# Optimization experiments

Hardware: AMD Instinct MI355X
Metric: run time of the kernel (lower is better)

## Reference

```python
import jax, jax.numpy as jnp
import numpy as np

E = 1024
H = 16
DH = E // H
EPS = 1e-8
GRAM_W = 1.5


def _gram_scores(q, k1, k2):
    # q: [BH, L, D], k1/k2: [BH, S, D] -> [BH, L, S]
    ll = jnp.sum(q * q, -1)[:, :, None]          # [BH, L, 1]
    vv = jnp.sum(k1 * k1, -1)[:, None, :]        # [BH, 1, S]
    aa = jnp.sum(k2 * k2, -1)[:, None, :]
    va = jnp.sum(k1 * k2, -1)[:, None, :]
    lv = jnp.einsum('bld,bsd->bls', q, k1)
    la = jnp.einsum('bld,bsd->bls', q, k2)
    det = ll * (vv * aa - va * va) - lv * (lv * aa - la * va) + la * (lv * va - la * vv)
    return -jnp.sqrt(jnp.clip(det, EPS, None))


def setup_inputs() -> dict:
    key = jax.random.key(0)
    ks = jax.random.split(key, 20)
    L, B, S = 512, 4, 1024
    inp = {
        'query': jax.random.normal(ks[0], (L, B, E), jnp.float32),
        'mod1': jax.random.normal(ks[1], (S, B, E), jnp.float32),
        'mod2': jax.random.normal(ks[2], (S, B, E), jnp.float32),
    }
    # Linear params stored as [in, out] (y = x @ W + b), 8 linears
    names = ['q', 'k1', 'k2', 'v1', 'v2', 'g1', 'g2', 'o']
    for i, n in enumerate(names):
        inp[n + '_w'] = jax.random.normal(ks[3 + 2 * i], (E, E), jnp.float32) * 0.02
        inp[n + '_b'] = jax.random.normal(ks[4 + 2 * i], (E,), jnp.float32) * 0.02
    return inp


def reference(query, mod1, mod2,
              q_w, q_b, k1_w, k1_b, k2_w, k2_b, v1_w, v1_b, v2_w, v2_b,
              g1_w, g1_b, g2_w, g2_b, o_w, o_b):
    L, B, _ = query.shape
    S = mod1.shape[0]
    scaling = DH ** -0.5

    def lin(x, w, b):
        return x @ w + b

    def split_heads(x, n):  # [n, B, E] -> [B*H, n, DH]
        return x.reshape(n, B * H, DH).transpose(1, 0, 2)

    q = split_heads(lin(query, q_w, q_b) * scaling, L)
    k1 = split_heads(lin(mod1, k1_w, k1_b), S)
    k2 = split_heads(lin(mod2, k2_w, k2_b), S)
    v1 = split_heads(lin(mod1, v1_w, v1_b), S)
    v2 = split_heads(lin(mod2, v2_w, v2_b), S)

    w1 = jnp.einsum('bld,bsd->bls', q, k1)
    w2 = jnp.einsum('bld,bsd->bls', q, k2)
    gram = _gram_scores(q, k1, k2)
    logits = GRAM_W * gram + w1 + w2          # [BH, L, S]
    attn = jax.nn.softmax(logits, axis=-1)

    def merge_heads(x):  # [B*H, L, DH] -> [L, B, E]
        return x.transpose(1, 0, 2).reshape(L, B, E)

    out1 = merge_heads(jnp.einsum('bls,bsd->bld', attn, v1))
    out2 = merge_heads(jnp.einsum('bls,bsd->bld', attn, v2))
    gate1 = jax.nn.sigmoid(lin(query, g1_w, g1_b))
    gate2 = jax.nn.sigmoid(lin(query, g2_w, g2_b))
    attn_output = lin((out1 * gate1 + out2 * gate2) / 2.0, o_w, o_b)
    avg_weights = attn.reshape(B, H, L, S).mean(axis=1)
    return attn_output, avg_weights
```

## Files before the change

kernel.cpp:

```cpp
#include <hip/hip_runtime.h>
#include <cstddef>
#include <cstdint>

typedef unsigned short ushort_t;
typedef unsigned int uint_t;
typedef __attribute__((ext_vector_type(8))) short short8;
typedef __attribute__((ext_vector_type(4))) float f32x4;

#define EDIM 1024
#define NHEAD 16
#define HDIM 64
#define NB 4
#define LQ 512
#define SK 1024
#define BHD 64

__device__ __forceinline__ ushort_t f2b(float f) {
    uint_t u = __float_as_uint(f);
    return (ushort_t)((u + 0x7fffu + ((u >> 16) & 1u)) >> 16);
}
__device__ __forceinline__ float b2f(ushort_t b) {
    return __uint_as_float(((uint_t)b) << 16);
}

__device__ __forceinline__ void gload_lds16(const void* g, void* l) {
    __builtin_amdgcn_global_load_lds((const __attribute__((address_space(1))) void*)g,
                                     (__attribute__((address_space(3))) void*)l, 16, 0, 0);
}

struct MegaArgs {
    const ushort_t *qx, *m1h, *m1l, *m2h, *m2l;
    const ushort_t *Wqg, *Wkv1, *Wkv2, *Wk1l, *Wk2l;
    const float *q_b, *k1_b, *k2_b, *v1_b, *v2_b, *g1_b, *g2_b;
    float *K1f, *K2f;
    ushort_t *V1b, *V2b, *Qb, *G1b, *G2b;
};

__global__ __launch_bounds__(256, 2)
void mega_gemm(MegaArgs a)
{
    __shared__ ushort_t As[128 * 64];
    __shared__ ushort_t Bs[128 * 64];
    const int tid = threadIdx.x;
    const int wave = tid >> 6, lane = tid & 63;
    const int ln = lane & 15, lq = lane >> 4;
    const int wm = wave & 1, wn = wave >> 1;
    const int mrl = lane >> 3;
    const int lswz = (lane & 7) ^ mrl;

    const int id = blockIdx.x;
    f32x4 zero = {0.f, 0.f, 0.f, 0.f};

    if (id < 512) {
        const int kind = id >> 8;
        const int t = id & 255;
        const int u = t >> 3;
        const int col0 = (u >> 2) * 128;
        const int row0 = ((t & 7) * 4 + (u & 3)) * 128;
        const ushort_t* Ah  = kind ? a.m2h : a.m1h;
        const ushort_t* Alo = kind ? a.m2l : a.m1l;
        const ushort_t* Bh  = kind ? a.Wkv2 : a.Wkv1;
        const ushort_t* Blo = kind ? a.Wk2l : a.Wk1l;
        const float* bias = kind ? a.k2_b : a.k1_b;

        f32x4 acc[4][4];
#pragma unroll
        for (int i = 0; i < 4; ++i)
#pragma unroll
            for (int j = 0; j < 4; ++j) acc[i][j] = zero;

        const int ksub = (lswz & 3) * 8;
        const ushort_t* Asrc = (lswz & 4) ? Alo : Ah;
        const ushort_t* Bsrc = (lswz & 4) ? Blo : Bh;

        for (int kk = 0; kk < 1024; kk += 32) {
            __syncthreads();
#pragma unroll
            for (int j = 0; j < 4; ++j) {
                const int mr = (wave * 4 + j) * 8 + mrl;
                gload_lds16(Asrc + (size_t)(row0 + mr) * 1024 + kk + ksub,
                            (void*)(As + (wave * 4 + j) * 512));
                gload_lds16(Bsrc + (size_t)(col0 + mr) * 1024 + kk + ksub,
                            (void*)(Bs + (wave * 4 + j) * 512));
            }
            __syncthreads();
            short8 ah[4], alv[4], bh[4], blv[4];
#pragma unroll
            for (int i = 0; i < 4; ++i) {
                const int ml = wm * 64 + i * 16 + ln;
                const int pa = (lq ^ (ml & 7)) * 8;
                ah[i]  = *(const short8*)(As + ml * 64 + pa);
                alv[i] = *(const short8*)(As + ml * 64 + (pa ^ 32));
                const int nl = wn * 64 + i * 16 + ln;
                const int pb = (lq ^ (nl & 7)) * 8;
                bh[i]  = *(const short8*)(Bs + nl * 64 + pb);
                blv[i] = *(const short8*)(Bs + nl * 64 + (pb ^ 32));
            }
#pragma unroll
            for (int i = 0; i < 4; ++i)
#pragma unroll
                for (int j = 0; j < 4; ++j)
                    acc[i][j] = __builtin_amdgcn_mfma_f32_16x16x32_bf16(ah[i], bh[j], acc[i][j], 0, 0, 0);
#pragma unroll
            for (int i = 0; i < 4; ++i)
#pragma unroll
                for (int j = 0; j < 4; ++j)
                    acc[i][j] = __builtin_amdgcn_mfma_f32_16x16x32_bf16(ah[i], blv[j], acc[i][j], 0, 0, 0);
#pragma unroll
            for (int i = 0; i < 4; ++i)
#pragma unroll
                for (int j = 0; j < 4; ++j)
                    acc[i][j] = __builtin_amdgcn_mfma_f32_16x16x32_bf16(alv[i], bh[j], acc[i][j], 0, 0, 0);
        }

        float* Y = kind ? a.K2f : a.K1f;
#pragma unroll
        for (int i = 0; i < 4; ++i) {
#pragma unroll
            for (int r = 0; r < 4; ++r) {
                const int row = row0 + wm * 64 + i * 16 + lq * 4 + r;
#pragma unroll
                for (int j = 0; j < 4; ++j) {
                    const int col = col0 + wn * 64 + j * 16 + ln;
                    const float v = acc[i][j][r] + bias[col];
                    const int s = row >> 2, b = row & 3, h = col >> 6, d = col & 63;
                    Y[(((size_t)(b * 16 + h)) * 1024 + s) * 64 + d] = v;
                }
            }
        }
        return;
    }

    int kind, row0, col0;
    const ushort_t *A, *B;
    const float* bias;
    if (id < 1024) {
        int t = id - 512; kind = 2 + (t >> 8); t &= 255;
        const int u = t >> 3;
        col0 = (u >> 2) * 128;
        row0 = ((t & 7) * 4 + (u & 3)) * 128;
        A = (kind == 2) ? a.m1h : a.m2h;
        B = ((kind == 2) ? a.Wkv1 : a.Wkv2) + (size_t)1024 * 1024;
        bias = (kind == 2) ? a.v1_b : a.v2_b;
    } else {
        const int t = id - 1024; kind = 4;
        const int u = t >> 3;
        const int c = (t & 7) * 3 + (u >> 4);
        const int rr = u & 15;
        col0 = c * 128; row0 = rr * 128;
        A = a.qx; B = a.Wqg;
        const int seg = c >> 3;
        bias = (seg == 0) ? a.q_b : ((seg == 1) ? a.g1_b : a.g2_b);
    }

    f32x4 acc[4][4];
#pragma unroll
    for (int i = 0; i < 4; ++i)
#pragma unroll
        for (int j = 0; j < 4; ++j) acc[i][j] = zero;

    for (int kk = 0; kk < 1024; kk += 64) {
        __syncthreads();
#pragma unroll
        for (int j = 0; j < 4; ++j) {
            const int mr = (wave * 4 + j) * 8 + mrl;
            gload_lds16(A + (size_t)(row0 + mr) * 1024 + kk + lswz * 8,
                        (void*)(As + (wave * 4 + j) * 512));
            gload_lds16(B + (size_t)(col0 + mr) * 1024 + kk + lswz * 8,
                        (void*)(Bs + (wave * 4 + j) * 512));
        }
        __syncthreads();
#pragma unroll
        for (int sub = 0; sub < 2; ++sub) {
            short8 af[4], bfv[4];
#pragma unroll
            for (int i = 0; i < 4; ++i) {
                const int ml = wm * 64 + i * 16 + ln;
                af[i] = *(const short8*)(As + ml * 64 + (((sub * 4 + lq) ^ (ml & 7)) * 8));
                const int nl = wn * 64 + i * 16 + ln;
                bfv[i] = *(const short8*)(Bs + nl * 64 + (((sub * 4 + lq) ^ (nl & 7)) * 8));
            }
#pragma unroll
            for (int i = 0; i < 4; ++i)
#pragma unroll
                for (int j = 0; j < 4; ++j)
                    acc[i][j] = __builtin_amdgcn_mfma_f32_16x16x32_bf16(af[i], bfv[j], acc[i][j], 0, 0, 0);
        }
    }

#pragma unroll
    for (int i = 0; i < 4; ++i) {
#pragma unroll
        for (int r = 0; r < 4; ++r) {
            const int row = row0 + wm * 64 + i * 16 + lq * 4 + r;
#pragma unroll
            for (int j = 0; j < 4; ++j) {
                const int col = col0 + wn * 64 + j * 16 + ln;
                const int lc = col & 1023;
                float v = acc[i][j][r] + bias[lc];
                if (kind <= 3) {
                    const int s = row >> 2, b = row & 3, h = lc >> 6, d = lc & 63;
                    ushort_t* Y = (kind == 2) ? a.V1b : a.V2b;
                    Y[(((size_t)(b * 16 + h)) * 1024 + s) * 64 + d] = f2b(v);
                } else {
                    const int seg = col >> 10;
                    if (seg == 0) {
                        v *= 0.125f;
                        const int s = row >> 2, b = row & 3, h = lc >> 6, d = lc & 63;
                        a.Qb[(((size_t)(b * 16 + h)) * 512 + s) * 64 + d] = f2b(v);
                    } else {
                        v = 1.0f / (1.0f + __expf(-v));
                        ushort_t* Y = (seg == 1) ? a.G1b : a.G2b;
                        Y[(size_t)row * 1024 + lc] = f2b(v);
                    }
                }
            }
        }
    }
}

struct CastArgs {
    const float* q; const float* m1; const float* m2;
    ushort_t* qx; ushort_t* m1h; ushort_t* m1l; ushort_t* m2h; ushort_t* m2l;
    const float* wsrc[8];
    ushort_t* whi[8];
    ushort_t* wlo[8];
};

__global__ __launch_bounds__(256)
void casts_kernel(CastArgs a)
{
    __shared__ float T[64][65];
    const int id = blockIdx.x;
    const int tid = threadIdx.x;
    if (id < 1024) {
        const size_t i = ((size_t)id * 256 + tid) * 8;
        float4 x = *(const float4*)(a.q + i);
        float4 y = *(const float4*)(a.q + i + 4);
        ushort_t o[8] = {f2b(x.x), f2b(x.y), f2b(x.z), f2b(x.w), f2b(y.x), f2b(y.y), f2b(y.z), f2b(y.w)};
        *(uint4*)( (void*)(a.qx + i) ) = *(const uint4*)o;
    } else if (id < 5120) {
        const int t = id - 1024;
        const int which = t >> 11;
        const float* x = which ? a.m2 : a.m1;
        ushort_t* yh = which ? a.m2h : a.m1h;
        ushort_t* yl = which ? a.m2l : a.m1l;
        const size_t i = ((size_t)(t & 2047) * 256 + tid) * 8;
        float v[8];
        *(float4*)v = *(const float4*)(x + i);
        *(float4*)(v + 4) = *(const float4*)(x + i + 4);
        ushort_t oh[8], ol[8];
#pragma unroll
        for (int k = 0; k < 8; ++k) {
            oh[k] = f2b(v[k]);
            ol[k] = f2b(v[k] - b2f(oh[k]));
        }
        *(uint4*)( (void*)(yh + i) ) = *(const uint4*)oh;
        *(uint4*)( (void*)(yl + i) ) = *(const uint4*)ol;
    } else {
        const int t = id - 5120;
        const int z = t >> 8, x = t & 15, y = (t >> 4) & 15;
        const float* W = a.wsrc[z];
        ushort_t* Th = a.whi[z];
        ushort_t* Tl = a.wlo[z];
        const int k0 = x * 64, n0 = y * 64;
        const int r = tid >> 2, cg = (tid & 3) * 16;
#pragma unroll
        for (int u = 0; u < 4; ++u) {
            float4 v = *(const float4*)(W + (size_t)(k0 + r) * 1024 + n0 + cg + u * 4);
            T[r][cg + u * 4 + 0] = v.x; T[r][cg + u * 4 + 1] = v.y;
            T[r][cg + u * 4 + 2] = v.z; T[r][cg + u * 4 + 3] = v.w;
        }
        __syncthreads();
        ushort_t oh[16], ol[16];
#pragma unroll
        for (int u = 0; u < 16; ++u) {
            float v = T[cg + u][r];
            oh[u] = f2b(v);
            ol[u] = f2b(v - b2f(oh[u]));
        }
        ushort_t* dh = Th + (size_t)(n0 + r) * 1024 + k0 + cg;
        *(uint4*)( (void*)dh ) = *(const uint4*)oh;
        *(uint4*)( (void*)(dh + 8) ) = *(const uint4*)(oh + 8);
        if (Tl) {
            ushort_t* dl = Tl + (size_t)(n0 + r) * 1024 + k0 + cg;
            *(uint4*)( (void*)dl ) = *(const uint4*)ol;
            *(uint4*)( (void*)(dl + 8) ) = *(const uint4*)(ol + 8);
        }
    }
}

__global__ __launch_bounds__(256)
void prep_kernel(const float* __restrict__ K1f, const float* __restrict__ K2f,
                 ushort_t* __restrict__ K1b, ushort_t* __restrict__ K2b,
                 float* __restrict__ vv, float* __restrict__ aa,
                 float* __restrict__ va2, float* __restrict__ gg,
                 const ushort_t* __restrict__ Qb, float* __restrict__ ll,
                 const ushort_t* __restrict__ V1b, const ushort_t* __restrict__ V2b,
                 ushort_t* __restrict__ V1t, ushort_t* __restrict__ V2t)
{
    __shared__ float T[64][65];
    const int id = blockIdx.x;
    const int tid = threadIdx.x;
    const int wave = tid >> 6, lane = tid & 63;
    if (id < 16384) {
        const int row = id * 4 + wave;
        const float x1 = K1f[(size_t)row * 64 + lane];
        const float x2 = K2f[(size_t)row * 64 + lane];
        K1b[(size_t)row * 64 + lane] = f2b(x1);
        K2b[(size_t)row * 64 + lane] = f2b(x2);
        float s1 = x1 * x1, s2 = x2 * x2, s3 = x1 * x2;
#pragma unroll
        for (int o = 1; o < 64; o <<= 1) {
            s1 += __shfl_xor(s1, o);
            s2 += __shfl_xor(s2, o);
            s3 += __shfl_xor(s3, o);
        }
        if (lane == 0) {
            vv[row] = s1; aa[row] = s2;
            va2[row] = 2.0f * s3;
            gg[row] = s1 * s2 - s3 * s3;
        }
    } else if (id < 24576) {
        const int row = (id - 16384) * 4 + wave;
        const float x = b2f(Qb[(size_t)row * 64 + lane]);
        float s = x * x;
#pragma unroll
        for (int o = 1; o < 64; o <<= 1) s += __shfl_xor(s, o);
        if (lane == 0) ll[row] = s;
    } else {
        const int t = id - 24576;
        const int z = t >> 10, bh = (t >> 4) & 63, s0 = (t & 15) * 64;
        const ushort_t* S = z ? V2b : V1b;
        ushort_t* D = z ? V2t : V1t;
        const int r = tid >> 2, cg = (tid & 3) * 16;
        ushort_t buf[16];
        const ushort_t* sp = S + ((size_t)bh * 1024 + s0 + r) * 64 + cg;
        *(uint4*)buf = *(const uint4*)sp;
        *(uint4*)(buf + 8) = *(const uint4*)(sp + 8);
#pragma unroll
        for (int u = 0; u < 16; ++u) T[r][cg + u] = b2f(buf[u]);
        __syncthreads();
        ushort_t o[16];
#pragma unroll
        for (int u = 0; u < 16; ++u) o[u] = f2b(T[cg + u][r]);
        ushort_t* d = D + ((size_t)bh * 64 + r) * 1024 + s0 + cg;
        *(uint4*)( (void*)d ) = *(const uint4*)o;
        *(uint4*)( (void*)(d + 8) ) = *(const uint4*)(o + 8);
    }
}

__global__ __launch_bounds__(256, 2)
void attn_fused(const ushort_t* __restrict__ Qb, const ushort_t* __restrict__ K1b,
                const ushort_t* __restrict__ K2b, const float* __restrict__ ll,
                const float* __restrict__ vv, const float* __restrict__ aa,
                const float* __restrict__ va2, const float* __restrict__ gg,
                ushort_t* __restrict__ attn, float* __restrict__ C)
{
    __shared__ ushort_t Qs[64 * 64];
    __shared__ ushort_t K1s[128 * 64];
    __shared__ ushort_t K2s[128 * 64];
    __shared__ float vvS[1024], aaS[1024], vaS[1024], ggS[1024], llS[64];
    const int tid = threadIdx.x;
    const int wave = tid >> 6, lane = tid & 63;
    const int ln = lane & 15, lq = lane >> 4;
    const int mrl = lane >> 3;
    const int cswz = (lane & 7) ^ mrl;
    const float L2E = 1.44269504f;

    const int id = blockIdx.x;
    const int bh = (id & 7) * 8 + ((id >> 3) & 7);
    const int l0 = (id >> 6) * 64;

    for (int i = tid; i < 1024; i += 256) {
        vvS[i] = vv[(size_t)bh * 1024 + i];
        aaS[i] = aa[(size_t)bh * 1024 + i];
        vaS[i] = va2[(size_t)bh * 1024 + i];
        ggS[i] = gg[(size_t)bh * 1024 + i];
    }
    if (tid < 64) llS[tid] = ll[(size_t)bh * 512 + l0 + tid];
#pragma unroll
    for (int j = 0; j < 2; ++j) {
        const int mr = (wave * 2 + j) * 8 + mrl;
        gload_lds16(Qb + ((size_t)bh * 512 + l0 + mr) * 64 + cswz * 8,
                    (void*)(Qs + (wave * 2 + j) * 512));
    }

    const int ml = wave * 16 + ln;
    const size_t rb = (size_t)bh * 512 + l0 + wave * 16 + lq * 4;

    float m_run[4], s_run[4];
#pragma unroll
    for (int r = 0; r < 4; ++r) { m_run[r] = -3.0e38f; s_run[r] = 0.f; }
    float mt[8][4];

#pragma unroll
    for (int t = 0; t < 8; ++t) {
        const int s0 = t * 128;
        __syncthreads();
#pragma unroll
        for (int j = 0; j < 4; ++j) {
            const int mr = (wave * 4 + j) * 8 + mrl;
            gload_lds16(K1b + ((size_t)bh * 1024 + s0 + mr) * 64 + cswz * 8,
                        (void*)(K1s + (wave * 4 + j) * 512));
            gload_lds16(K2b + ((size_t)bh * 1024 + s0 + mr) * 64 + cswz * 8,
                        (void*)(K2s + (wave * 4 + j) * 512));
        }
        __syncthreads();
        f32x4 zero = {0.f, 0.f, 0.f, 0.f};
        f32x4 lv[8], la[8];
#pragma unroll
        for (int j = 0; j < 8; ++j) { lv[j] = zero; la[j] = zero; }
#pragma unroll
        for (int sub = 0; sub < 2; ++sub) {
            const short8 qf = *(const short8*)(Qs + ml * 64 + (((sub * 4 + lq) ^ (ml & 7)) * 8));
#pragma unroll
            for (int j = 0; j < 8; ++j) {
                const int nl = j * 16 + ln;
                const short8 k1f = *(const short8*)(K1s + nl * 64 + (((sub * 4 + lq) ^ (nl & 7)) * 8));
                const short8 k2f = *(const short8*)(K2s + nl * 64 + (((sub * 4 + lq) ^ (nl & 7)) * 8));
                lv[j] = __builtin_amdgcn_mfma_f32_16x16x32_bf16(qf, k1f, lv[j], 0, 0, 0);
                la[j] = __builtin_amdgcn_mfma_f32_16x16x32_bf16(qf, k2f, la[j], 0, 0, 0);
            }
        }
        float lgt[8][4];
#pragma unroll
        for (int j = 0; j < 8; ++j) {
            const int c = s0 + j * 16 + ln;
            const float VV = vvS[c], AA = aaS[c], VA2 = vaS[c], GB = ggS[c];
#pragma unroll
            for (int r = 0; r < 4; ++r) {
                const float LL = llS[wave * 16 + lq * 4 + r];
                const float LV = lv[j][r], LA = la[j][r];
                float det = LL * GB;
                det = fmaf(-AA, LV * LV, det);
                det = fmaf(VA2, LV * LA, det);
                det = fmaf(-VV, LA * LA, det);
                det = fmaxf(det, 1e-8f);
                lgt[j][r] = (LV + LA) - 1.5f * sqrtf(det);
            }
        }
        float tmax[4];
#pragma unroll
        for (int r = 0; r < 4; ++r) tmax[r] = lgt[0][r];
#pragma unroll
        for (int j = 1; j < 8; ++j)
#pragma unroll
            for (int r = 0; r < 4; ++r) tmax[r] = fmaxf(tmax[r], lgt[j][r]);
#pragma unroll
        for (int r = 0; r < 4; ++r) {
#pragma unroll
            for (int o = 1; o < 16; o <<= 1) tmax[r] = fmaxf(tmax[r], __shfl_xor(tmax[r], o));
        }
        float mn[4], nm[4], ps[4];
#pragma unroll
        for (int r = 0; r < 4; ++r) {
            mn[r] = fmaxf(m_run[r], tmax[r]);
            nm[r] = -mn[r] * L2E;
            ps[r] = 0.f;
        }
#pragma unroll
        for (int j = 0; j < 8; ++j) {
            const int col = s0 + j * 16 + ln;
            float p[4];
#pragma unroll
            for (int r = 0; r < 4; ++r) {
                p[r] = exp2f(fmaf(lgt[j][r], L2E, nm[r]));
                ps[r] += p[r];
            }
            attn[(rb + 0) * 1024 + col] = f2b(p[0]);
            attn[(rb + 1) * 1024 + col] = f2b(p[1]);
            attn[(rb + 2) * 1024 + col] = f2b(p[2]);
            attn[(rb + 3) * 1024 + col] = f2b(p[3]);
        }
#pragma unroll
        for (int r = 0; r < 4; ++r) {
            s_run[r] = s_run[r] * __expf(m_run[r] - mn[r]) + ps[r];
            m_run[r] = mn[r];
            mt[t][r] = mn[r];
        }
    }

    float inv[4];
#pragma unroll
    for (int r = 0; r < 4; ++r) {
        float s = s_run[r];
#pragma unroll
        for (int o = 1; o < 16; o <<= 1) s += __shfl_xor(s, o);
        inv[r] = 1.0f / s;
    }

    if (ln == 0) {
#pragma unroll
        for (int t = 0; t < 8; ++t) {
#pragma unroll
            for (int r = 0; r < 4; ++r)
                C[(rb + r) * 8 + t] = __expf(mt[t][r] - m_run[r]) * inv[r];
        }
    }
}

__global__ __launch_bounds__(256, 2)
void pv_gate_kernel(const ushort_t* __restrict__ attn, const ushort_t* __restrict__ V1t,
                    const ushort_t* __restrict__ V2t, const ushort_t* __restrict__ G1,
                    const ushort_t* __restrict__ G2, const float* __restrict__ C,
                    ushort_t* __restrict__ tmpb, float* __restrict__ avg)
{
    __shared__ ushort_t Ps[128 * 64];
    __shared__ ushort_t V1s[64 * 64];
    __shared__ ushort_t V2s[64 * 64];
    const int tid = threadIdx.x;

    if (blockIdx.x >= 256) {
        const int t = blockIdx.x - 256;
        const int b = t >> 9, l = t & 511;
        const int c0 = tid * 4;
        const int tt = tid >> 5;
        float s0_ = 0.f, s1_ = 0.f, s2_ = 0.f, s3_ = 0.f;
#pragma unroll
        for (int h = 0; h < 16; ++h) {
            const size_t row = ((size_t)(b * 16 + h)) * 512 + l;
            const float ch = C[row * 8 + tt];
            const ushort_t* p = attn + row * 1024 + c0;
            ushort_t u[4];
            *(uint2*)u = *(const uint2*)p;
            s0_ = fmaf(b2f(u[0]), ch, s0_); s1_ = fmaf(b2f(u[1]), ch, s1_);
            s2_ = fmaf(b2f(u[2]), ch, s2_); s3_ = fmaf(b2f(u[3]), ch, s3_);
        }
        float4 o = {s0_ * 0.0625f, s1_ * 0.0625f, s2_ * 0.0625f, s3_ * 0.0625f};
        *(float4*)(avg + ((size_t)(b * 512 + l)) * 1024 + c0) = o;
        return;
    }

    const int wave = tid >> 6, lane = tid & 63;
    const int ln = lane & 15, lq = lane >> 4;
    const int bh = blockIdx.x >> 2;
    const int l0 = (blockIdx.x & 3) * 128;
    const int cswz = (lane & 7) ^ ((lane >> 3) & 7);
    const int mrl = lane >> 3;
    const int bq = bh >> 4, h = bh & 15;

    f32x4 zero = {0.f, 0.f, 0.f, 0.f};
    f32x4 acc1[2][4], acc2[2][4], tacc1[2][4], tacc2[2][4];
#pragma unroll
    for (int i = 0; i < 2; ++i)
#pragma unroll
        for (int j = 0; j < 4; ++j) {
            acc1[i][j] = zero; acc2[i][j] = zero;
            tacc1[i][j] = zero; tacc2[i][j] = zero;
        }

    for (int s0 = 0; s0 < 1024; s0 += 64) {
        __syncthreads();
#pragma unroll
        for (int j = 0; j < 4; ++j) {
            const int mr = (wave * 4 + j) * 8 + mrl;
            gload_lds16(attn + ((size_t)bh * 512 + l0 + mr) * 1024 + s0 + cswz * 8,
                        (void*)(Ps + (wave * 4 + j) * 512));
        }
#pragma unroll
        for (int j = 0; j < 2; ++j) {
            const int mv = (wave * 2 + j) * 8 + mrl;
            gload_lds16(V1t + ((size_t)bh * 64 + mv) * 1024 + s0 + cswz * 8,
                        (void*)(V1s + (wave * 2 + j) * 512));
            gload_lds16(V2t + ((size_t)bh * 64 + mv) * 1024 + s0 + cswz * 8,
                        (void*)(V2s + (wave * 2 + j) * 512));
        }
        __syncthreads();
#pragma unroll
        for (int sub = 0; sub < 2; ++sub) {
            short8 af[2], b1f[4], b2f_[4];
#pragma unroll
            for (int i = 0; i < 2; ++i) {
                const int ml = wave * 32 + i * 16 + ln;
                af[i] = *(const short8*)(Ps + ml * 64 + (((sub * 4 + lq) ^ (ml & 7)) * 8));
            }
#pragma unroll
            for (int j = 0; j < 4; ++j) {
                const int nl = j * 16 + ln;
                b1f[j] = *(const short8*)(V1s + nl * 64 + (((sub * 4 + lq) ^ (nl & 7)) * 8));
                b2f_[j] = *(const short8*)(V2s + nl * 64 + (((sub * 4 + lq) ^ (nl & 7)) * 8));
            }
#pragma unroll
            for (int i = 0; i < 2; ++i)
#pragma unroll
                for (int j = 0; j < 4; ++j) {
                    tacc1[i][j] = __builtin_amdgcn_mfma_f32_16x16x32_bf16(af[i], b1f[j], tacc1[i][j], 0, 0, 0);
                    tacc2[i][j] = __builtin_amdgcn_mfma_f32_16x16x32_bf16(af[i], b2f_[j], tacc2[i][j], 0, 0, 0);
                }
        }
        if (s0 & 64) {
            const int tt = s0 >> 7;
#pragma unroll
            for (int i = 0; i < 2; ++i) {
#pragma unroll
                for (int r = 0; r < 4; ++r) {
                    const int l = l0 + wave * 32 + i * 16 + lq * 4 + r;
                    const float c = C[((size_t)bh * 512 + l) * 8 + tt];
#pragma unroll
                    for (int j = 0; j < 4; ++j) {
                        acc1[i][j][r] = fmaf(c, tacc1[i][j][r], acc1[i][j][r]);
                        acc2[i][j][r] = fmaf(c, tacc2[i][j][r], acc2[i][j][r]);
                    }
                }
            }
#pragma unroll
            for (int i = 0; i < 2; ++i)
#pragma unroll
                for (int j = 0; j < 4; ++j) { tacc1[i][j] = zero; tacc2[i][j] = zero; }
        }
    }

#pragma unroll
    for (int i = 0; i < 2; ++i) {
#pragma unroll
        for (int r = 0; r < 4; ++r) {
            const int l = l0 + wave * 32 + i * 16 + lq * 4 + r;
#pragma unroll
            for (int j = 0; j < 4; ++j) {
                const int d = j * 16 + ln;
                const size_t addr = ((size_t)l * 4 + bq) * 1024 + h * 64 + d;
                const float v = 0.5f * (acc1[i][j][r] * b2f(G1[addr]) + acc2[i][j][r] * b2f(G2[addr]));
                tmpb[addr] = f2b(v);
            }
        }
    }
}

__global__ __launch_bounds__(256, 2)
void gemm_o64(const ushort_t* __restrict__ A, const ushort_t* __restrict__ B,
              const float* __restrict__ bias, float* __restrict__ Y)
{
    __shared__ ushort_t As[64 * 64];
    __shared__ ushort_t Bs[128 * 64];
    const int tid = threadIdx.x;
    const int wave = tid >> 6, lane = tid & 63;
    const int ln = lane & 15, lq = lane >> 4;
    const int row0 = blockIdx.y * 64, col0 = blockIdx.x * 128;
    const int wm = wave & 1, wn = wave >> 1;
    const int cswz = (lane & 7) ^ ((lane >> 3) & 7);
    const int mrl = lane >> 3;

    f32x4 zero = {0.f, 0.f, 0.f, 0.f};
    f32x4 acc[2][4];
#pragma unroll
    for (int i = 0; i < 2; ++i)
#pragma unroll
        for (int j = 0; j < 4; ++j) acc[i][j] = zero;

    for (int kk = 0; kk < 1024; kk += 64) {
        __syncthreads();
#pragma unroll
        for (int j = 0; j < 2; ++j) {
            const int mr = (wave * 2 + j) * 8 + mrl;
            gload_lds16(A + (size_t)(row0 + mr) * 1024 + kk + cswz * 8,
                        (void*)(As + (wave * 2 + j) * 512));
        }
#pragma unroll
        for (int j = 0; j < 4; ++j) {
            const int mr = (wave * 4 + j) * 8 + mrl;
            gload_lds16(B + (size_t)(col0 + mr) * 1024 + kk + cswz * 8,
                        (void*)(Bs + (wave * 4 + j) * 512));
        }
        __syncthreads();
#pragma unroll
        for (int sub = 0; sub < 2; ++sub) {
            short8 af[2], bfv[4];
#pragma unroll
            for (int i = 0; i < 2; ++i) {
                const int ml = wm * 32 + i * 16 + ln;
                af[i] = *(const short8*)(As + ml * 64 + (((sub * 4 + lq) ^ (ml & 7)) * 8));
            }
#pragma unroll
            for (int j = 0; j < 4; ++j) {
                const int nl = wn * 64 + j * 16 + ln;
                bfv[j] = *(const short8*)(Bs + nl * 64 + (((sub * 4 + lq) ^ (nl & 7)) * 8));
            }
#pragma unroll
            for (int i = 0; i < 2; ++i)
#pragma unroll
                for (int j = 0; j < 4; ++j)
                    acc[i][j] = __builtin_amdgcn_mfma_f32_16x16x32_bf16(af[i], bfv[j], acc[i][j], 0, 0, 0);
        }
    }

#pragma unroll
    for (int i = 0; i < 2; ++i) {
#pragma unroll
        for (int r = 0; r < 4; ++r) {
            const int row = row0 + wm * 32 + i * 16 + lq * 4 + r;
#pragma unroll
            for (int j = 0; j < 4; ++j) {
                const int col = col0 + wn * 64 + j * 16 + ln;
                Y[(size_t)row * 1024 + col] = acc[i][j][r] + bias[col];
            }
        }
    }
}

extern "C" void kernel_launch(void* const* d_in, const int* in_sizes, int n_in,
                              void* d_out, int out_size, void* d_ws, size_t ws_size,
                              hipStream_t stream)
{
    const float* query = (const float*)d_in[0];
    const float* mod1  = (const float*)d_in[1];
    const float* mod2  = (const float*)d_in[2];
    const float* q_w  = (const float*)d_in[3];  const float* q_b  = (const float*)d_in[4];
    const float* k1_w = (const float*)d_in[5];  const float* k1_b = (const float*)d_in[6];
    const float* k2_w = (const float*)d_in[7];  const float* k2_b = (const float*)d_in[8];
    const float* v1_w = (const float*)d_in[9];  const float* v1_b = (const float*)d_in[10];
    const float* v2_w = (const float*)d_in[11]; const float* v2_b = (const float*)d_in[12];
    const float* g1_w = (const float*)d_in[13]; const float* g1_b = (const float*)d_in[14];
    const float* g2_w = (const float*)d_in[15]; const float* g2_b = (const float*)d_in[16];
    const float* o_w  = (const float*)d_in[17]; const float* o_b  = (const float*)d_in[18];
    float* out = (float*)d_out;

    const size_t MB = 1u << 20;
    char* w = (char*)d_ws;
    ushort_t* Wqg  = (ushort_t*)(w + 0 * MB);
    ushort_t* Wkv1 = (ushort_t*)(w + 6 * MB);
    ushort_t* Wkv2 = (ushort_t*)(w + 10 * MB);
    ushort_t* Wo   = (ushort_t*)(w + 14 * MB);
    ushort_t* Wk1l = (ushort_t*)(w + 16 * MB);
    ushort_t* Wk2l = (ushort_t*)(w + 18 * MB);
    ushort_t* qx   = (ushort_t*)(w + 20 * MB);
    ushort_t* tmpb = qx;
    ushort_t* Qb   = (ushort_t*)(w + 24 * MB);
    ushort_t* K1b  = (ushort_t*)(w + 28 * MB);
    ushort_t* K2b  = (ushort_t*)(w + 36 * MB);
    ushort_t* V1t  = (ushort_t*)(w + 44 * MB);
    ushort_t* V2t  = (ushort_t*)(w + 52 * MB);
    ushort_t* G1b  = (ushort_t*)(w + 60 * MB);
    ushort_t* G2b  = (ushort_t*)(w + 64 * MB);
    float* ll  = (float*)(w + 68 * MB);
    float* vv  = (float*)(w + 68 * MB + 256 * 1024);
    float* aa  = (float*)(w + 68 * MB + 512 * 1024);
    float* va2 = (float*)(w + 68 * MB + 768 * 1024);
    float* gg  = (float*)(w + 68 * MB + 1024 * 1024);
    float* Cs  = (float*)(w + 70 * MB);
    ushort_t* attn = (ushort_t*)(w + 78 * MB);
    ushort_t* m1h = (ushort_t*)(w + 78 * MB);
    ushort_t* m2h = (ushort_t*)(w + 86 * MB);
    ushort_t* m1l = (ushort_t*)(w + 94 * MB);
    ushort_t* m2l = (ushort_t*)(w + 102 * MB);
    float* K1f = (float*)(w + 110 * MB);
    float* K2f = (float*)(w + 126 * MB);
    ushort_t* V1b = (ushort_t*)(w + 142 * MB);
    ushort_t* V2b = (ushort_t*)(w + 150 * MB);

    CastArgs ca;
    ca.q = query; ca.m1 = mod1; ca.m2 = mod2;
    ca.qx = qx; ca.m1h = m1h; ca.m1l = m1l; ca.m2h = m2h; ca.m2l = m2l;
    const float* srcs[8] = {q_w, g1_w, g2_w, k1_w, v1_w, k2_w, v2_w, o_w};
    ushort_t* his[8] = {Wqg, Wqg + (size_t)1024 * 1024, Wqg + (size_t)2048 * 1024,
                        Wkv1, Wkv1 + (size_t)1024 * 1024, Wkv2, Wkv2 + (size_t)1024 * 1024, Wo};
    ushort_t* los[8] = {nullptr, nullptr, nullptr, Wk1l, nullptr, Wk2l, nullptr, nullptr};
    for (int i = 0; i < 8; ++i) { ca.wsrc[i] = srcs[i]; ca.whi[i] = his[i]; ca.wlo[i] = los[i]; }
    casts_kernel<<<7168, 256, 0, stream>>>(ca);

    MegaArgs ma;
    ma.qx = qx; ma.m1h = m1h; ma.m1l = m1l; ma.m2h = m2h; ma.m2l = m2l;
    ma.Wqg = Wqg; ma.Wkv1 = Wkv1; ma.Wkv2 = Wkv2; ma.Wk1l = Wk1l; ma.Wk2l = Wk2l;
    ma.q_b = q_b; ma.k1_b = k1_b; ma.k2_b = k2_b; ma.v1_b = v1_b; ma.v2_b = v2_b;
    ma.g1_b = g1_b; ma.g2_b = g2_b;
    ma.K1f = K1f; ma.K2f = K2f; ma.V1b = V1b; ma.V2b = V2b;
    ma.Qb = Qb; ma.G1b = G1b; ma.G2b = G2b;
    mega_gemm<<<1408, 256, 0, stream>>>(ma);

    prep_kernel<<<26624, 256, 0, stream>>>(K1f, K2f, K1b, K2b, vv, aa, va2, gg,
                                           Qb, ll, V1b, V2b, V1t, V2t);

    attn_fused<<<512, 256, 0, stream>>>(Qb, K1b, K2b, ll, vv, aa, va2, gg, attn, Cs);

    pv_gate_kernel<<<2304, 256, 0, stream>>>(attn, V1t, V2t, G1b, G2b, Cs, tmpb,
                                             out + (size_t)LQ * NB * EDIM);

    gemm_o64<<<dim3(8, 32), 256, 0, stream>>>(tmpb, Wo, o_b, out);
}
```

Baseline: 361.1 us.

## Widen cast/prep per-thread work, drop gg buffer, raise attn occupancy hint

The cast kernel now handles 16 elements per thread instead of 8, and prep_kernel reduces each row with 16 lanes using float4 loads instead of a full wave of scalar loads. This cuts launch block counts and the cost of shuffle reductions. The precomputed gg buffer is removed: attn_fused recomputes the Gram term from vv, aa and va2 in registers, and per-row ll values are loaded into registers instead of LDS. The launch bound for attn_fused rises to 3 blocks per SM, which may force register spills in a kernel that is already heavy.

New measurement: 534.6 us. 1.48x slower.

```diff
diff --git a/kernel.cpp b/kernel.cpp
--- a/kernel.cpp
+++ b/kernel.cpp
@@ -233,32 +233,40 @@
     __shared__ float T[64][65];
     const int id = blockIdx.x;
     const int tid = threadIdx.x;
-    if (id < 1024) {
-        const size_t i = ((size_t)id * 256 + tid) * 8;
-        float4 x = *(const float4*)(a.q + i);
-        float4 y = *(const float4*)(a.q + i + 4);
-        ushort_t o[8] = {f2b(x.x), f2b(x.y), f2b(x.z), f2b(x.w), f2b(y.x), f2b(y.y), f2b(y.z), f2b(y.w)};
+    if (id < 512) {
+        const size_t i = ((size_t)id * 256 + tid) * 16;
+        float v[16];
+#pragma unroll
+        for (int c = 0; c < 4; ++c)
+            *(float4*)(v + c * 4) = *(const float4*)(a.q + i + c * 4);
+        ushort_t o[16];
+#pragma unroll
+        for (int k = 0; k < 16; ++k) o[k] = f2b(v[k]);
         *(uint4*)( (void*)(a.qx + i) ) = *(const uint4*)o;
-    } else if (id < 5120) {
-        const int t = id - 1024;
-        const int which = t >> 11;
+        *(uint4*)( (void*)(a.qx + i + 8) ) = *(const uint4*)(o + 8);
+    } else if (id < 2560) {
+        const int t = id - 512;
+        const int which = t >> 10;
         const float* x = which ? a.m2 : a.m1;
         ushort_t* yh = which ? a.m2h : a.m1h;
         ushort_t* yl = which ? a.m2l : a.m1l;
-        const size_t i = ((size_t)(t & 2047) * 256 + tid) * 8;
-        float v[8];
-        *(float4*)v = *(const float4*)(x + i);
-        *(float4*)(v + 4) = *(const float4*)(x + i + 4);
-        ushort_t oh[8], ol[8];
-#pragma unroll
-        for (int k = 0; k < 8; ++k) {
+        const size_t i = ((size_t)(t & 1023) * 256 + tid) * 16;
+        float v[16];
+#pragma unroll
+        for (int c = 0; c < 4; ++c)
+            *(float4*)(v + c * 4) = *(const float4*)(x + i + c * 4);
+        ushort_t oh[16], ol[16];
+#pragma unroll
+        for (int k = 0; k < 16; ++k) {
             oh[k] = f2b(v[k]);
             ol[k] = f2b(v[k] - b2f(oh[k]));
         }
         *(uint4*)( (void*)(yh + i) ) = *(const uint4*)oh;
+        *(uint4*)( (void*)(yh + i + 8) ) = *(const uint4*)(oh + 8);
         *(uint4*)( (void*)(yl + i) ) = *(const uint4*)ol;
+        *(uint4*)( (void*)(yl + i + 8) ) = *(const uint4*)(ol + 8);
     } else {
-        const int t = id - 5120;
+        const int t = id - 2560;
         const int z = t >> 8, x = t & 15, y = (t >> 4) & 15;
         const float* W = a.wsrc[z];
         ushort_t* Th = a.whi[z];
@@ -294,7 +302,7 @@
 void prep_kernel(const float* __restrict__ K1f, const float* __restrict__ K2f,
                  ushort_t* __restrict__ K1b, ushort_t* __restrict__ K2b,
                  float* __restrict__ vv, float* __restrict__ aa,
-                 float* __restrict__ va2, float* __restrict__ gg,
+                 float* __restrict__ va2,
                  const ushort_t* __restrict__ Qb, float* __restrict__ ll,
                  const ushort_t* __restrict__ V1b, const ushort_t* __restrict__ V2b,
                  ushort_t* __restrict__ V1t, ushort_t* __restrict__ V2t)
@@ -302,34 +310,40 @@
     __shared__ float T[64][65];
     const int id = blockIdx.x;
     const int tid = threadIdx.x;
-    const int wave = tid >> 6, lane = tid & 63;
-    if (id < 16384) {
-        const int row = id * 4 + wave;
-        const float x1 = K1f[(size_t)row * 64 + lane];
-        const float x2 = K2f[(size_t)row * 64 + lane];
-        K1b[(size_t)row * 64 + lane] = f2b(x1);
-        K2b[(size_t)row * 64 + lane] = f2b(x2);
-        float s1 = x1 * x1, s2 = x2 * x2, s3 = x1 * x2;
-#pragma unroll
-        for (int o = 1; o < 64; o <<= 1) {
+    if (id < 4096) {
+        const int row = id * 16 + (tid >> 4);
+        const int g = tid & 15;
+        const float4 x1 = *(const float4*)(K1f + (size_t)row * 64 + g * 4);
+        const float4 x2 = *(const float4*)(K2f + (size_t)row * 64 + g * 4);
+        ushort_t o1[4] = {f2b(x1.x), f2b(x1.y), f2b(x1.z), f2b(x1.w)};
+        ushort_t o2[4] = {f2b(x2.x), f2b(x2.y), f2b(x2.z), f2b(x2.w)};
+        *(uint2*)( (void*)(K1b + (size_t)row * 64 + g * 4) ) = *(const uint2*)o1;
+        *(uint2*)( (void*)(K2b + (size_t)row * 64 + g * 4) ) = *(const uint2*)o2;
+        float s1 = x1.x * x1.x + x1.y * x1.y + x1.z * x1.z + x1.w * x1.w;
+        float s2 = x2.x * x2.x + x2.y * x2.y + x2.z * x2.z + x2.w * x2.w;
+        float s3 = x1.x * x2.x + x1.y * x2.y + x1.z * x2.z + x1.w * x2.w;
+#pragma unroll
+        for (int o = 1; o < 16; o <<= 1) {
             s1 += __shfl_xor(s1, o);
             s2 += __shfl_xor(s2, o);
             s3 += __shfl_xor(s3, o);
         }
-        if (lane == 0) {
+        if (g == 0) {
             vv[row] = s1; aa[row] = s2;
             va2[row] = 2.0f * s3;
-            gg[row] = s1 * s2 - s3 * s3;
-        }
-    } else if (id < 24576) {
-        const int row = (id - 16384) * 4 + wave;
-        const float x = b2f(Qb[(size_t)row * 64 + lane]);
-        float s = x * x;
-#pragma unroll
-        for (int o = 1; o < 64; o <<= 1) s += __shfl_xor(s, o);
-        if (lane == 0) ll[row] = s;
+        }
+    } else if (id < 6144) {
+        const int row = (id - 4096) * 16 + (tid >> 4);
+        const int g = tid & 15;
+        ushort_t u[4];
+        *(uint2*)u = *(const uint2*)(Qb + (size_t)row * 64 + g * 4);
+        const float a0 = b2f(u[0]), a1 = b2f(u[1]), a2 = b2f(u[2]), a3 = b2f(u[3]);
+        float s = a0 * a0 + a1 * a1 + a2 * a2 + a3 * a3;
+#pragma unroll
+        for (int o = 1; o < 16; o <<= 1) s += __shfl_xor(s, o);
+        if (g == 0) ll[row] = s;
     } else {
-        const int t = id - 24576;
+        const int t = id - 6144;
         const int z = t >> 10, bh = (t >> 4) & 63, s0 = (t & 15) * 64;
         const ushort_t* S = z ? V2b : V1b;
         ushort_t* D = z ? V2t : V1t;
@@ -350,17 +364,17 @@
     }
 }
 
-__global__ __launch_bounds__(256, 2)
+__global__ __launch_bounds__(256, 3)
 void attn_fused(const ushort_t* __restrict__ Qb, const ushort_t* __restrict__ K1b,
                 const ushort_t* __restrict__ K2b, const float* __restrict__ ll,
                 const float* __restrict__ vv, const float* __restrict__ aa,
-                const float* __restrict__ va2, const float* __restrict__ gg,
+                const float* __restrict__ va2,
                 ushort_t* __restrict__ attn, float* __restrict__ C)
 {
     __shared__ ushort_t Qs[64 * 64];
     __shared__ ushort_t K1s[128 * 64];
     __shared__ ushort_t K2s[128 * 64];
-    __shared__ float vvS[1024], aaS[1024], vaS[1024], ggS[1024], llS[64];
+    __shared__ float vvS[1024], aaS[1024], vaS[1024];
     const int tid = threadIdx.x;
     const int wave = tid >> 6, lane = tid & 63;
     const int ln = lane & 15, lq = lane >> 4;
@@ -376,9 +390,7 @@
         vvS[i] = vv[(size_t)bh * 1024 + i];
         aaS[i] = aa[(size_t)bh * 1024 + i];
         vaS[i] = va2[(size_t)bh * 1024 + i];
-        ggS[i] = gg[(size_t)bh * 1024 + i];
-    }
-    if (tid < 64) llS[tid] = ll[(size_t)bh * 512 + l0 + tid];
+    }
 #pragma unroll
     for (int j = 0; j < 2; ++j) {
         const int mr = (wave * 2 + j) * 8 + mrl;
@@ -388,6 +400,9 @@
 
     const int ml = wave * 16 + ln;
     const size_t rb = (size_t)bh * 512 + l0 + wave * 16 + lq * 4;
+    float LLr[4];
+#pragma unroll
+    for (int r = 0; r < 4; ++r) LLr[r] = ll[rb + r];
 
     float m_run[4], s_run[4];
 #pragma unroll
@@ -427,12 +442,12 @@
 #pragma unroll
         for (int j = 0; j < 8; ++j) {
             const int c = s0 + j * 16 + ln;
-            const float VV = vvS[c], AA = aaS[c], VA2 = vaS[c], GB = ggS[c];
+            const float VV = vvS[c], AA = aaS[c], VA2 = vaS[c];
+            const float GB = fmaf(-0.25f * VA2, VA2, VV * AA);
 #pragma unroll
             for (int r = 0; r < 4; ++r) {
-                const float LL = llS[wave * 16 + lq * 4 + r];
                 const float LV = lv[j][r], LA = la[j][r];
-                float det = LL * GB;
+                float det = LLr[r] * GB;
                 det = fmaf(-AA, LV * LV, det);
                 det = fmaf(VA2, LV * LA, det);
                 det = fmaf(-VV, LA * LA, det);
@@ -736,7 +751,6 @@
     float* vv  = (float*)(w + 68 * MB + 256 * 1024);
     float* aa  = (float*)(w + 68 * MB + 512 * 1024);
     float* va2 = (float*)(w + 68 * MB + 768 * 1024);
-    float* gg  = (float*)(w + 68 * MB + 1024 * 1024);
     float* Cs  = (float*)(w + 70 * MB);
     ushort_t* attn = (ushort_t*)(w + 78 * MB);
     ushort_t* m1h = (ushort_t*)(w + 78 * MB);
@@ -756,7 +770,7 @@
                         Wkv1, Wkv1 + (size_t)1024 * 1024, Wkv2, Wkv2 + (size_t)1024 * 1024, Wo};
     ushort_t* los[8] = {nullptr, nullptr, nullptr, Wk1l, nullptr, Wk2l, nullptr, nullptr};
     for (int i = 0; i < 8; ++i) { ca.wsrc[i] = srcs[i]; ca.whi[i] = his[i]; ca.wlo[i] = los[i]; }
-    casts_kernel<<<7168, 256, 0, stream>>>(ca);
+    casts_kernel<<<4608, 256, 0, stream>>>(ca);
 
     MegaArgs ma;
     ma.qx = qx; ma.m1h = m1h; ma.m1l = m1l; ma.m2h = m2h; ma.m2l = m2l;
@@ -767,10 +781,10 @@
     ma.Qb = Qb; ma.G1b = G1b; ma.G2b = G2b;
     mega_gemm<<<1408, 256, 0, stream>>>(ma);
 
-    prep_kernel<<<26624, 256, 0, stream>>>(K1f, K2f, K1b, K2b, vv, aa, va2, gg,
-                                           Qb, ll, V1b, V2b, V1t, V2t);
-
-    attn_fused<<<512, 256, 0, stream>>>(Qb, K1b, K2b, ll, vv, aa, va2, gg, attn, Cs);
+    prep_kernel<<<8192, 256, 0, stream>>>(K1f, K2f, K1b, K2b, vv, aa, va2,
+                                          Qb, ll, V1b, V2b, V1t, V2t);
+
+    attn_fused<<<512, 256, 0, stream>>>(Qb, K1b, K2b, ll, vv, aa, va2, attn, Cs);
 
     pv_gate_kernel<<<2304, 256, 0, stream>>>(attn, V1t, V2t, G1b, G2b, Cs, tmpb,
                                              out + (size_t)LQ * NB * EDIM);
```
